# Kernel optimization log

Hardware: AMD Instinct MI355X
Metric: run time of the kernel (lower is better)

Reference implementation:

```python
import jax, jax.numpy as jnp
import numpy as np

DIM = 1024
HID = 2816
E = 8
TOPK = 2
B, S = 4, 1024


def setup_inputs() -> dict:
    key = jax.random.key(0)
    k_x, k_g, k1, k2, k3 = jax.random.split(key, 5)
    scale_d = 1.0 / np.sqrt(DIM)
    scale_h = 1.0 / np.sqrt(HID)
    return {
        "x": jax.random.normal(k_x, (B, S, DIM), dtype=jnp.float32),
        "Wg": jax.random.normal(k_g, (E, DIM), dtype=jnp.float32) * scale_d,   # gate: Linear(dim, E), no bias
        "W1": jax.random.normal(k1, (E, HID, DIM), dtype=jnp.float32) * scale_d,  # swiglu gate proj
        "W3": jax.random.normal(k3, (E, HID, DIM), dtype=jnp.float32) * scale_d,  # swiglu up proj
        "W2": jax.random.normal(k2, (E, DIM, HID), dtype=jnp.float32) * scale_h,  # down proj
    }


def reference(x, Wg, W1, W3, W2):
    Bsz, Ssz, D = x.shape
    xt = x.reshape(Bsz * Ssz, D)                        # [T, D]

    # Gating: top-k over expert scores, softmax over selected logits
    scores = xt @ Wg.T                                   # [T, E]
    top_vals, top_idx = jax.lax.top_k(scores, TOPK)      # [T, K]
    weights = jax.nn.softmax(top_vals, axis=-1)          # [T, K]

    # Dense grouped SwiGLU: run every expert on every token (vectorized),
    # then gather the top-k expert outputs per token.
    h1 = jnp.einsum('td,ehd->teh', xt, W1)               # [T, E, H]
    h3 = jnp.einsum('td,ehd->teh', xt, W3)               # [T, E, H]
    expert_out = jnp.einsum('teh,edh->ted', jax.nn.silu(h1) * h3, W2)  # [T, E, D]

    # Gather per-token selected experts and combine with gate weights
    idx = top_idx[:, :, None]                            # [T, K, 1]
    sel = jnp.take_along_axis(expert_out, idx, axis=1)   # [T, K, D]
    out = jnp.sum(sel * weights[:, :, None], axis=1)     # [T, D]
    return out.reshape(Bsz, Ssz, D)
```

## Files before the change

kernel.cpp:

```cpp
#include <hip/hip_runtime.h>
#include <hip/hip_bf16.h>

#define DIM  1024
#define HID  2816
#define NE   8
#define NTOK 4096
#define NPAIR 8192
#define CAP  8192

#define NT_UP (HID / 128)
#define MT    (CAP / 128)
#define NT_DN (DIM / 128)
#define NWG_UP (NE * NT_UP * MT)
#define NWG_DN (NE * NT_DN * MT)

typedef __bf16 bf16x8 __attribute__((ext_vector_type(8)));
typedef float f32x4 __attribute__((ext_vector_type(4)));

#define OFF_CNT  0
#define OFF_LIST 1024
#define OFF_WP   (OFF_LIST + NE*CAP*4)
#define OFF_H1   (OFF_WP + NPAIR*4)
#define OFF_XB   ((size_t)1 << 20)
#define OFF_W1B  ((size_t)10 << 20)
#define OFF_W3B  ((size_t)57 << 20)
#define OFF_H2   ((size_t)106 << 20)
#define WS_NEED  (OFF_H2 + (size_t)NPAIR * HID * 2)

#define GLB(p) ((const __attribute__((address_space(1))) void*)(p))
#define LDS(p) ((__attribute__((address_space(3))) void*)(p))

__global__ __launch_bounds__(64) void gate_kernel(
    const float* __restrict__ x, const float* __restrict__ Wg,
    int* __restrict__ counts, int* __restrict__ list, float* __restrict__ wpair,
    __bf16* __restrict__ xb) {
  int t = blockIdx.x;
  int lane = threadIdx.x;
  const float* xp = x + (size_t)t * DIM;
  float xr[16];
#pragma unroll
  for (int i = 0; i < 16; ++i) xr[i] = xp[lane + 64 * i];
  if (xb) {
    __bf16* xo = xb + (size_t)t * DIM;
#pragma unroll
    for (int i = 0; i < 16; ++i) xo[lane + 64 * i] = (__bf16)xr[i];
  }
  float s[NE];
#pragma unroll
  for (int e = 0; e < NE; ++e) {
    const float* wp = Wg + e * DIM;
    float acc = 0.f;
#pragma unroll
    for (int i = 0; i < 16; ++i) acc += xr[i] * wp[lane + 64 * i];
#pragma unroll
    for (int off = 32; off >= 1; off >>= 1) acc += __shfl_xor(acc, off, 64);
    s[e] = acc;
  }
  if (lane == 0) {
    int i0 = 0; float b0 = s[0];
#pragma unroll
    for (int e = 1; e < NE; ++e) if (s[e] > b0) { b0 = s[e]; i0 = e; }
    int i1 = -1; float b1 = -1e30f;
#pragma unroll
    for (int e = 0; e < NE; ++e) if (e != i0 && s[e] > b1) { b1 = s[e]; i1 = e; }
    float e1 = __expf(b1 - b0);
    float w0 = 1.f / (1.f + e1);
    float w1 = e1 * w0;
    int s0 = atomicAdd(&counts[i0], 1);
    list[i0 * CAP + s0] = 2 * t;
    wpair[2 * t] = w0;
    int s1 = atomicAdd(&counts[i1], 1);
    list[i1 * CAP + s1] = 2 * t + 1;
    wpair[2 * t + 1] = w1;
  }
}

__global__ __launch_bounds__(256) void cvt_kernel(
    const float* __restrict__ src, __bf16* __restrict__ dst) {
  size_t i = (((size_t)blockIdx.x * 256) + threadIdx.x) * 8;
  float4 f0 = *(const float4*)(src + i);
  float4 f1 = *(const float4*)(src + i + 4);
  bf16x8 v;
  v[0] = (__bf16)f0.x; v[1] = (__bf16)f0.y; v[2] = (__bf16)f0.z; v[3] = (__bf16)f0.w;
  v[4] = (__bf16)f1.x; v[5] = (__bf16)f1.y; v[6] = (__bf16)f1.z; v[7] = (__bf16)f1.w;
  *(bf16x8*)(dst + i) = v;
}


__global__ __launch_bounds__(256, 2) void up4_kernel(
    const __bf16* __restrict__ xb, const __bf16* __restrict__ w1b,
    const __bf16* __restrict__ w3b, const int* __restrict__ counts,
    const int* __restrict__ list, const float* __restrict__ wpair,
    __bf16* __restrict__ Hbuf) {
  int bid = blockIdx.x;
  int g = (bid & 7) * (NWG_UP / 8) + (bid >> 3);
  int e = g / (NT_UP * MT);
  int rr0 = g % (NT_UP * MT);
  int cnt = counts[e];
  int m0 = (rr0 % MT) * 128;
  if (m0 >= cnt) return;
  int h0 = (rr0 / MT) * 128;

  __shared__ __bf16 As[128 * 64];
  __shared__ __bf16 B1s[128 * 64];
  __shared__ __bf16 B3s[128 * 64];

  int tid = threadIdx.x;
  int lane = tid & 63;
  int w = tid >> 6;
  int cl = lane & 15, hi = lane >> 4;
  int wr = w >> 1, wc = w & 1;
  int l8 = lane >> 3, cc = lane & 7;

  const __bf16* asrc[4];
  const __bf16* b1src[4];
  const __bf16* b3src[4];
#pragma unroll
  for (int i = 0; i < 4; ++i) {
    int r = (w * 4 + i) * 8 + l8;
    int csel = (cc ^ (r & 7)) * 8;
    int mrow = m0 + r; if (mrow > cnt - 1) mrow = cnt - 1;
    int p = list[e * CAP + mrow];
    asrc[i]  = xb + (size_t)(p >> 1) * DIM + csel;
    b1src[i] = w1b + ((size_t)e * HID + h0 + r) * DIM + csel;
    b3src[i] = w3b + ((size_t)e * HID + h0 + r) * DIM + csel;
  }

  f32x4 acc1[4][4] = {};
  f32x4 acc3[4][4] = {};

  for (int k0 = 0; k0 < DIM; k0 += 64) {
#pragma unroll
    for (int i = 0; i < 4; ++i) {
      int q = (w * 4 + i) * 1024;
      __builtin_amdgcn_global_load_lds(GLB(asrc[i] + k0),  LDS((char*)As  + q), 16, 0, 0);
      __builtin_amdgcn_global_load_lds(GLB(b1src[i] + k0), LDS((char*)B1s + q), 16, 0, 0);
      __builtin_amdgcn_global_load_lds(GLB(b3src[i] + k0), LDS((char*)B3s + q), 16, 0, 0);
    }
    __syncthreads();
#pragma unroll
    for (int ks = 0; ks < 2; ++ks) {
      int c = hi + ks * 4;
      bf16x8 a[4], bb1[4], bb3[4];
#pragma unroll
      for (int mi = 0; mi < 4; ++mi) {
        int r = wr * 64 + mi * 16 + cl;
        a[mi] = *(const bf16x8*)((const char*)As + r * 128 + ((c ^ (r & 7)) * 16));
      }
#pragma unroll
      for (int ni = 0; ni < 4; ++ni) {
        int r = wc * 64 + ni * 16 + cl;
        bb1[ni] = *(const bf16x8*)((const char*)B1s + r * 128 + ((c ^ (r & 7)) * 16));
        bb3[ni] = *(const bf16x8*)((const char*)B3s + r * 128 + ((c ^ (r & 7)) * 16));
      }
#pragma unroll
      for (int mi = 0; mi < 4; ++mi)
#pragma unroll
        for (int ni = 0; ni < 4; ++ni) {
          acc1[mi][ni] = __builtin_amdgcn_mfma_f32_16x16x32_bf16(a[mi], bb1[ni], acc1[mi][ni], 0, 0, 0);
          acc3[mi][ni] = __builtin_amdgcn_mfma_f32_16x16x32_bf16(a[mi], bb3[ni], acc3[mi][ni], 0, 0, 0);
        }
    }
    __syncthreads();
  }

#pragma unroll
  for (int mi = 0; mi < 4; ++mi) {
#pragma unroll
    for (int rr = 0; rr < 4; ++rr) {
      int m = m0 + wr * 64 + mi * 16 + hi * 4 + rr;
      if (m < cnt) {
        int p = list[e * CAP + m];
        float wgt = wpair[p];
        __bf16* hp = Hbuf + (size_t)p * HID + h0 + wc * 64 + cl;
#pragma unroll
        for (int ni = 0; ni < 4; ++ni) {
          float v1 = acc1[mi][ni][rr], v3 = acc3[mi][ni][rr];
          float gv = (v1 / (1.f + __expf(-v1))) * v3 * wgt;
          hp[ni * 16] = (__bf16)gv;
        }
      }
    }
  }
}

__global__ __launch_bounds__(256, 2) void down4_kernel(
    const __bf16* __restrict__ Hbuf, const __bf16* __restrict__ w2b,
    const int* __restrict__ counts, const int* __restrict__ list,
    __bf16* __restrict__ Obuf) {
  int bid = blockIdx.x;
  int g = (bid & 7) * (NWG_DN / 8) + (bid >> 3);
  int e = g / (NT_DN * MT);
  int rr0 = g % (NT_DN * MT);
  int cnt = counts[e];
  int m0 = (rr0 % MT) * 128;
  if (m0 >= cnt) return;
  int d0 = (rr0 / MT) * 128;

  __shared__ __bf16 As[128 * 64];
  __shared__ __bf16 Bs[128 * 64];

  int tid = threadIdx.x;
  int lane = tid & 63;
  int w = tid >> 6;
  int cl = lane & 15, hi = lane >> 4;
  int wr = w >> 1, wc = w & 1;
  int l8 = lane >> 3, cc = lane & 7;

  const __bf16* asrc[4];
  const __bf16* bsrc[4];
#pragma unroll
  for (int i = 0; i < 4; ++i) {
    int r = (w * 4 + i) * 8 + l8;
    int csel = (cc ^ (r & 7)) * 8;
    int mrow = m0 + r; if (mrow > cnt - 1) mrow = cnt - 1;
    int p = list[e * CAP + mrow];
    asrc[i] = Hbuf + (size_t)p * HID + csel;
    bsrc[i] = w2b + ((size_t)e * DIM + d0 + r) * HID + csel;
  }

  f32x4 acc[4][4] = {};

  for (int k0 = 0; k0 < HID; k0 += 64) {
#pragma unroll
    for (int i = 0; i < 4; ++i) {
      int q = (w * 4 + i) * 1024;
      __builtin_amdgcn_global_load_lds(GLB(asrc[i] + k0), LDS((char*)As + q), 16, 0, 0);
      __builtin_amdgcn_global_load_lds(GLB(bsrc[i] + k0), LDS((char*)Bs + q), 16, 0, 0);
    }
    __syncthreads();
#pragma unroll
    for (int ks = 0; ks < 2; ++ks) {
      int c = hi + ks * 4;
      bf16x8 a[4], b[4];
#pragma unroll
      for (int mi = 0; mi < 4; ++mi) {
        int r = wr * 64 + mi * 16 + cl;
        a[mi] = *(const bf16x8*)((const char*)As + r * 128 + ((c ^ (r & 7)) * 16));
      }
#pragma unroll
      for (int ni = 0; ni < 4; ++ni) {
        int r = wc * 64 + ni * 16 + cl;
        b[ni] = *(const bf16x8*)((const char*)Bs + r * 128 + ((c ^ (r & 7)) * 16));
      }
#pragma unroll
      for (int mi = 0; mi < 4; ++mi)
#pragma unroll
        for (int ni = 0; ni < 4; ++ni)
          acc[mi][ni] = __builtin_amdgcn_mfma_f32_16x16x32_bf16(a[mi], b[ni], acc[mi][ni], 0, 0, 0);
    }
    __syncthreads();
  }

#pragma unroll
  for (int mi = 0; mi < 4; ++mi) {
#pragma unroll
    for (int rr = 0; rr < 4; ++rr) {
      int m = m0 + wr * 64 + mi * 16 + hi * 4 + rr;
      if (m < cnt) {
        int p = list[e * CAP + m];
        __bf16* op = Obuf + (size_t)p * DIM + d0 + wc * 64 + cl;
#pragma unroll
        for (int ni = 0; ni < 4; ++ni)
          op[ni * 16] = (__bf16)acc[mi][ni][rr];
      }
    }
  }
}

__global__ __launch_bounds__(256) void combine_kernel(
    const __bf16* __restrict__ Obuf, float* __restrict__ out) {
  size_t j = (((size_t)blockIdx.x * 256) + threadIdx.x) * 8;
  size_t t = j >> 10;
  bf16x8 a = *(const bf16x8*)(Obuf + j + t * DIM);
  bf16x8 b = *(const bf16x8*)(Obuf + j + t * DIM + DIM);
  float4 o0, o1;
  o0.x = (float)a[0] + (float)b[0]; o0.y = (float)a[1] + (float)b[1];
  o0.z = (float)a[2] + (float)b[2]; o0.w = (float)a[3] + (float)b[3];
  o1.x = (float)a[4] + (float)b[4]; o1.y = (float)a[5] + (float)b[5];
  o1.z = (float)a[6] + (float)b[6]; o1.w = (float)a[7] + (float)b[7];
  *(float4*)(out + j) = o0;
  *(float4*)(out + j + 4) = o1;
}

__device__ __forceinline__ void cvt_store16(__bf16* dst, const float* src) {
#pragma unroll
  for (int j = 0; j < 2; ++j) {
    float4 f0 = *(const float4*)(src + j * 8);
    float4 f1 = *(const float4*)(src + j * 8 + 4);
    bf16x8 v;
    v[0] = (__bf16)f0.x; v[1] = (__bf16)f0.y; v[2] = (__bf16)f0.z; v[3] = (__bf16)f0.w;
    v[4] = (__bf16)f1.x; v[5] = (__bf16)f1.y; v[6] = (__bf16)f1.z; v[7] = (__bf16)f1.w;
    *(bf16x8*)(dst + j * 8) = v;
  }
}

__global__ __launch_bounds__(256) void up_kernel(
    const float* __restrict__ x, const float* __restrict__ W1,
    const float* __restrict__ W3, const int* __restrict__ counts,
    const int* __restrict__ list, __bf16* __restrict__ Hbuf) {
  int e = blockIdx.z;
  int cnt = counts[e];
  int m0 = blockIdx.y * 64;
  if (m0 >= cnt) return;
  int h0 = blockIdx.x * 64;

  __shared__ __bf16 As[64][72];
  __shared__ __bf16 B1s[64][72];
  __shared__ __bf16 B3s[64][72];

  int tid = threadIdx.x;
  int r = tid >> 2;
  int cs = (tid & 3) * 16;

  const float* asrc = nullptr;
  int mrow = m0 + r;
  if (mrow < cnt) {
    int p = list[e * CAP + mrow];
    asrc = x + (size_t)(p >> 1) * DIM;
  }
  const float* b1src = W1 + ((size_t)e * HID + (h0 + r)) * DIM;
  const float* b3src = W3 + ((size_t)e * HID + (h0 + r)) * DIM;

  int lane = tid & 63;
  int w = tid >> 6;
  int wr = w >> 1, wc = w & 1;
  int cl = lane & 15, hi = lane >> 4;

  f32x4 acc1[2][2] = {};
  f32x4 acc3[2][2] = {};

  for (int k0 = 0; k0 < DIM; k0 += 64) {
    if (asrc) {
      cvt_store16(&As[r][cs], asrc + k0 + cs);
    } else {
      bf16x8 z = {};
      *(bf16x8*)&As[r][cs] = z;
      *(bf16x8*)&As[r][cs + 8] = z;
    }
    cvt_store16(&B1s[r][cs], b1src + k0 + cs);
    cvt_store16(&B3s[r][cs], b3src + k0 + cs);
    __syncthreads();
#pragma unroll
    for (int ks = 0; ks < 64; ks += 32) {
      bf16x8 a[2], b1f[2], b3f[2];
#pragma unroll
      for (int mi = 0; mi < 2; ++mi)
        a[mi] = *(const bf16x8*)&As[wr * 32 + mi * 16 + cl][ks + hi * 8];
#pragma unroll
      for (int ni = 0; ni < 2; ++ni) {
        b1f[ni] = *(const bf16x8*)&B1s[wc * 32 + ni * 16 + cl][ks + hi * 8];
        b3f[ni] = *(const bf16x8*)&B3s[wc * 32 + ni * 16 + cl][ks + hi * 8];
      }
#pragma unroll
      for (int mi = 0; mi < 2; ++mi)
#pragma unroll
        for (int ni = 0; ni < 2; ++ni) {
          acc1[mi][ni] = __builtin_amdgcn_mfma_f32_16x16x32_bf16(a[mi], b1f[ni], acc1[mi][ni], 0, 0, 0);
          acc3[mi][ni] = __builtin_amdgcn_mfma_f32_16x16x32_bf16(a[mi], b3f[ni], acc3[mi][ni], 0, 0, 0);
        }
    }
    __syncthreads();
  }

#pragma unroll
  for (int mi = 0; mi < 2; ++mi) {
#pragma unroll
    for (int rr = 0; rr < 4; ++rr) {
      int m = m0 + wr * 32 + mi * 16 + hi * 4 + rr;
      if (m < cnt) {
        int p = list[e * CAP + m];
        __bf16* hp = Hbuf + (size_t)p * HID + h0 + wc * 32 + cl;
#pragma unroll
        for (int ni = 0; ni < 2; ++ni) {
          float v1 = acc1[mi][ni][rr], v3 = acc3[mi][ni][rr];
          float gg = (v1 / (1.f + __expf(-v1))) * v3;
          hp[ni * 16] = (__bf16)gg;
        }
      }
    }
  }
}

__global__ __launch_bounds__(256) void down_kernel(
    const __bf16* __restrict__ Hbuf, const float* __restrict__ W2,
    const int* __restrict__ counts, const int* __restrict__ list,
    const float* __restrict__ wpair, float* __restrict__ out) {
  int e = blockIdx.z;
  int cnt = counts[e];
  int m0 = blockIdx.y * 64;
  if (m0 >= cnt) return;
  int d0 = blockIdx.x * 64;

  __shared__ __bf16 As[64][72];
  __shared__ __bf16 Bs[64][72];

  int tid = threadIdx.x;
  int r = tid >> 2;
  int cs = (tid & 3) * 16;

  const __bf16* asrc = nullptr;
  int mrow = m0 + r;
  if (mrow < cnt) {
    int p = list[e * CAP + mrow];
    asrc = Hbuf + (size_t)p * HID;
  }
  const float* bsrc = W2 + ((size_t)e * DIM + (d0 + r)) * HID;

  int lane = tid & 63;
  int w = tid >> 6;
  int wr = w >> 1, wc = w & 1;
  int cl = lane & 15, hi = lane >> 4;

  f32x4 acc[2][2] = {};

  for (int k0 = 0; k0 < HID; k0 += 64) {
    if (asrc) {
      *(bf16x8*)&As[r][cs]     = *(const bf16x8*)(asrc + k0 + cs);
      *(bf16x8*)&As[r][cs + 8] = *(const bf16x8*)(asrc + k0 + cs + 8);
    } else {
      bf16x8 z = {};
      *(bf16x8*)&As[r][cs] = z;
      *(bf16x8*)&As[r][cs + 8] = z;
    }
    cvt_store16(&Bs[r][cs], bsrc + k0 + cs);
    __syncthreads();
#pragma unroll
    for (int ks = 0; ks < 64; ks += 32) {
      bf16x8 a[2], b[2];
#pragma unroll
      for (int mi = 0; mi < 2; ++mi)
        a[mi] = *(const bf16x8*)&As[wr * 32 + mi * 16 + cl][ks + hi * 8];
#pragma unroll
      for (int ni = 0; ni < 2; ++ni)
        b[ni] = *(const bf16x8*)&Bs[wc * 32 + ni * 16 + cl][ks + hi * 8];
#pragma unroll
      for (int mi = 0; mi < 2; ++mi)
#pragma unroll
        for (int ni = 0; ni < 2; ++ni)
          acc[mi][ni] = __builtin_amdgcn_mfma_f32_16x16x32_bf16(a[mi], b[ni], acc[mi][ni], 0, 0, 0);
    }
    __syncthreads();
  }

#pragma unroll
  for (int mi = 0; mi < 2; ++mi) {
#pragma unroll
    for (int rr = 0; rr < 4; ++rr) {
      int m = m0 + wr * 32 + mi * 16 + hi * 4 + rr;
      if (m < cnt) {
        int p = list[e * CAP + m];
        int t = p >> 1;
        float wgt = wpair[p];
        float* op = out + (size_t)t * DIM + d0 + wc * 32 + cl;
#pragma unroll
        for (int ni = 0; ni < 2; ++ni)
          atomicAdd(&op[ni * 16], wgt * acc[mi][ni][rr]);
      }
    }
  }
}

extern "C" void kernel_launch(void* const* d_in, const int* in_sizes, int n_in,
                              void* d_out, int out_size, void* d_ws, size_t ws_size,
                              hipStream_t stream) {
  const float* x  = (const float*)d_in[0];
  const float* Wg = (const float*)d_in[1];
  const float* W1 = (const float*)d_in[2];
  const float* W3 = (const float*)d_in[3];
  const float* W2 = (const float*)d_in[4];
  float* out = (float*)d_out;

  char* ws = (char*)d_ws;
  int* counts  = (int*)(ws + OFF_CNT);
  int* list    = (int*)(ws + OFF_LIST);
  float* wpair = (float*)(ws + OFF_WP);

  hipMemsetAsync(counts, 0, 64, stream);

  if (ws_size >= WS_NEED) {
    __bf16* xb   = (__bf16*)(ws + OFF_XB);
    __bf16* w1b  = (__bf16*)(ws + OFF_W1B);
    __bf16* w3b  = (__bf16*)(ws + OFF_W3B);
    __bf16* Hbuf = (__bf16*)(ws + OFF_H2);
    __bf16* Obuf = (__bf16*)(ws + OFF_W3B);

    gate_kernel<<<NTOK, 64, 0, stream>>>(x, Wg, counts, list, wpair, xb);

    cvt_kernel<<<NE * HID * DIM / 2048, 256, 0, stream>>>(W1, w1b);
    cvt_kernel<<<NE * HID * DIM / 2048, 256, 0, stream>>>(W3, w3b);

    up4_kernel<<<NWG_UP, 256, 0, stream>>>(xb, w1b, w3b, counts, list, wpair, Hbuf);

    cvt_kernel<<<NE * DIM * HID / 2048, 256, 0, stream>>>(W2, w1b);

    down4_kernel<<<NWG_DN, 256, 0, stream>>>(Hbuf, w1b, counts, list, Obuf);

    combine_kernel<<<NTOK * DIM / 2048, 256, 0, stream>>>(Obuf, out);
  } else {
    hipMemsetAsync(d_out, 0, (size_t)out_size * sizeof(float), stream);
    __bf16* Hbuf = (__bf16*)(ws + OFF_H1);
    gate_kernel<<<NTOK, 64, 0, stream>>>(x, Wg, counts, list, wpair, nullptr);
    up_kernel<<<dim3(HID / 64, CAP / 64, NE), 256, 0, stream>>>(x, W1, W3, counts, list, Hbuf);
    down_kernel<<<dim3(DIM / 64, CAP / 64, NE), 256, 0, stream>>>(Hbuf, W2, counts, list, wpair, out);
  }
}
```

Before: 391.3 us.

## Fuse W1/W3 bf16 conversion into weight-stationary up kernel, triple-buffer down GEMM

The up projection now loads each expert's 16-row slice of fp32 W1/W3 once, converts it to bf16 in LDS, and loops over all token tiles of that expert, streaming the activations from global memory with register prefetch. This removes the two separate W1/W3 conversion passes and their bf16 copies. The down kernel uses 128x64 tiles with a three-stage global_load_lds pipeline using explicit waitcnt and barriers. In exchange, up tiles are small (16 columns), so MFMA reuse is low and activations are re-read from global for every h-slice.

```diff
diff --git a/kernel.cpp b/kernel.cpp
--- a/kernel.cpp
+++ b/kernel.cpp
@@ -8,12 +8,6 @@
 #define NPAIR 8192
 #define CAP  8192
 
-#define NT_UP (HID / 128)
-#define MT    (CAP / 128)
-#define NT_DN (DIM / 128)
-#define NWG_UP (NE * NT_UP * MT)
-#define NWG_DN (NE * NT_DN * MT)
-
 typedef __bf16 bf16x8 __attribute__((ext_vector_type(8)));
 typedef float f32x4 __attribute__((ext_vector_type(4)));
 
@@ -22,13 +16,20 @@
 #define OFF_WP   (OFF_LIST + NE*CAP*4)
 #define OFF_H1   (OFF_WP + NPAIR*4)
 #define OFF_XB   ((size_t)1 << 20)
-#define OFF_W1B  ((size_t)10 << 20)
-#define OFF_W3B  ((size_t)57 << 20)
-#define OFF_H2   ((size_t)106 << 20)
-#define WS_NEED  (OFF_H2 + (size_t)NPAIR * HID * 2)
+#define OFF_W2B  ((size_t)10 << 20)
+#define OFF_H2   ((size_t)57 << 20)
+#define OFF_OB   ((size_t)104 << 20)
+#define WS_NEED  (OFF_OB + (size_t)NPAIR * DIM * 2)
 
 #define GLB(p) ((const __attribute__((address_space(1))) void*)(p))
 #define LDS(p) ((__attribute__((address_space(3))) void*)(p))
+
+__device__ __forceinline__ bf16x8 pack8(float4 a, float4 b) {
+  bf16x8 v;
+  v[0] = (__bf16)a.x; v[1] = (__bf16)a.y; v[2] = (__bf16)a.z; v[3] = (__bf16)a.w;
+  v[4] = (__bf16)b.x; v[5] = (__bf16)b.y; v[6] = (__bf16)b.z; v[7] = (__bf16)b.w;
+  return v;
+}
 
 __global__ __launch_bounds__(64) void gate_kernel(
     const float* __restrict__ x, const float* __restrict__ Wg,
@@ -80,88 +81,205 @@
   size_t i = (((size_t)blockIdx.x * 256) + threadIdx.x) * 8;
   float4 f0 = *(const float4*)(src + i);
   float4 f1 = *(const float4*)(src + i + 4);
-  bf16x8 v;
-  v[0] = (__bf16)f0.x; v[1] = (__bf16)f0.y; v[2] = (__bf16)f0.z; v[3] = (__bf16)f0.w;
-  v[4] = (__bf16)f1.x; v[5] = (__bf16)f1.y; v[6] = (__bf16)f1.z; v[7] = (__bf16)f1.w;
-  *(bf16x8*)(dst + i) = v;
-}
-
-
-__global__ __launch_bounds__(256, 2) void up4_kernel(
-    const __bf16* __restrict__ xb, const __bf16* __restrict__ w1b,
-    const __bf16* __restrict__ w3b, const int* __restrict__ counts,
+  *(bf16x8*)(dst + i) = pack8(f0, f1);
+}
+
+__global__ __launch_bounds__(256) void up7_kernel(
+    const __bf16* __restrict__ xb, const float* __restrict__ W1,
+    const float* __restrict__ W3, const int* __restrict__ counts,
     const int* __restrict__ list, const float* __restrict__ wpair,
     __bf16* __restrict__ Hbuf) {
-  int bid = blockIdx.x;
-  int g = (bid & 7) * (NWG_UP / 8) + (bid >> 3);
-  int e = g / (NT_UP * MT);
-  int rr0 = g % (NT_UP * MT);
+  int g = blockIdx.x;
+  int e = g / (HID / 16);
+  int h0 = (g % (HID / 16)) * 16;
   int cnt = counts[e];
-  int m0 = (rr0 % MT) * 128;
-  if (m0 >= cnt) return;
-  int h0 = (rr0 / MT) * 128;
-
-  __shared__ __bf16 As[128 * 64];
-  __shared__ __bf16 B1s[128 * 64];
-  __shared__ __bf16 B3s[128 * 64];
+
+  __shared__ __bf16 B1s[16 * 1024];
+  __shared__ __bf16 B3s[16 * 1024];
 
   int tid = threadIdx.x;
   int lane = tid & 63;
   int w = tid >> 6;
   int cl = lane & 15, hi = lane >> 4;
+
+  {
+    int row = tid >> 4;
+    const float* w1p = W1 + ((size_t)e * HID + h0 + row) * DIM;
+    const float* w3p = W3 + ((size_t)e * HID + h0 + row) * DIM;
+#pragma unroll
+    for (int i = 0; i < 8; ++i) {
+      int c16 = (tid & 15) + 16 * i;
+      int dst = row * 2048 + ((c16 ^ (row & 7)) * 16);
+      float4 a0 = *(const float4*)(w1p + c16 * 8);
+      float4 a1 = *(const float4*)(w1p + c16 * 8 + 4);
+      *(bf16x8*)((char*)B1s + dst) = pack8(a0, a1);
+      float4 b0 = *(const float4*)(w3p + c16 * 8);
+      float4 b1v = *(const float4*)(w3p + c16 * 8 + 4);
+      *(bf16x8*)((char*)B3s + dst) = pack8(b0, b1v);
+    }
+  }
+  __syncthreads();
+
+  int nmt = (cnt + 127) >> 7;
+  const int* lste = list + e * CAP;
+
+  for (int mt = 0; mt < nmt; ++mt) {
+    int m0 = mt * 128;
+    size_t apos[2];
+#pragma unroll
+    for (int mi = 0; mi < 2; ++mi) {
+      int r = m0 + w * 32 + mi * 16 + cl;
+      if (r > cnt - 1) r = cnt - 1;
+      int p = lste[r];
+      apos[mi] = (size_t)(p >> 1) * DIM + hi * 8;
+    }
+
+    f32x4 acc1[2] = {};
+    f32x4 acc3[2] = {};
+
+    bf16x8 af[2][2][2];
+#pragma unroll
+    for (int kt = 0; kt < 2; ++kt)
+#pragma unroll
+      for (int mi = 0; mi < 2; ++mi)
+#pragma unroll
+        for (int ks = 0; ks < 2; ++ks)
+          af[kt][mi][ks] = *(const bf16x8*)(xb + apos[mi] + kt * 64 + ks * 32);
+
+#pragma unroll
+    for (int kt = 0; kt < 16; ++kt) {
+      int par = kt & 1;
+      bf16x8 b1f[2], b3f[2];
+#pragma unroll
+      for (int ks = 0; ks < 2; ++ks) {
+        int c16 = kt * 8 + ks * 4 + hi;
+        int off = cl * 2048 + ((c16 ^ (cl & 7)) * 16);
+        b1f[ks] = *(const bf16x8*)((const char*)B1s + off);
+        b3f[ks] = *(const bf16x8*)((const char*)B3s + off);
+      }
+#pragma unroll
+      for (int ks = 0; ks < 2; ++ks)
+#pragma unroll
+        for (int mi = 0; mi < 2; ++mi) {
+          acc1[mi] = __builtin_amdgcn_mfma_f32_16x16x32_bf16(af[par][mi][ks], b1f[ks], acc1[mi], 0, 0, 0);
+          acc3[mi] = __builtin_amdgcn_mfma_f32_16x16x32_bf16(af[par][mi][ks], b3f[ks], acc3[mi], 0, 0, 0);
+        }
+      if (kt + 2 < 16) {
+#pragma unroll
+        for (int mi = 0; mi < 2; ++mi)
+#pragma unroll
+          for (int ks = 0; ks < 2; ++ks)
+            af[par][mi][ks] = *(const bf16x8*)(xb + apos[mi] + (kt + 2) * 64 + ks * 32);
+      }
+    }
+
+#pragma unroll
+    for (int mi = 0; mi < 2; ++mi) {
+#pragma unroll
+      for (int rr = 0; rr < 4; ++rr) {
+        int m = m0 + w * 32 + mi * 16 + hi * 4 + rr;
+        if (m < cnt) {
+          int p = lste[m];
+          float wgt = wpair[p];
+          float v1 = acc1[mi][rr], v3 = acc3[mi][rr];
+          float gv = (v1 / (1.f + __expf(-v1))) * v3 * wgt;
+          Hbuf[(size_t)p * HID + h0 + cl] = (__bf16)gv;
+        }
+      }
+    }
+  }
+}
+
+__global__ __launch_bounds__(256, 2) void down6_kernel(
+    const __bf16* __restrict__ Hbuf, const __bf16* __restrict__ w2b,
+    const int* __restrict__ counts, const int* __restrict__ list,
+    __bf16* __restrict__ Obuf) {
+  int g = blockIdx.x;
+  int e = g >> 8;
+  int rem = g & 255;
+  int m0 = (rem & 15) * 128;
+  int d0 = (rem >> 4) * 64;
+  int cnt = counts[e];
+  if (m0 >= cnt) return;
+
+  __shared__ __bf16 As[3][128 * 64];
+  __shared__ __bf16 Bs[3][64 * 64];
+
+  int tid = threadIdx.x;
+  int lane = tid & 63;
+  int w = tid >> 6;
   int wr = w >> 1, wc = w & 1;
-  int l8 = lane >> 3, cc = lane & 7;
+  int cl = lane & 15, hi = lane >> 4;
 
   const __bf16* asrc[4];
-  const __bf16* b1src[4];
-  const __bf16* b3src[4];
-#pragma unroll
-  for (int i = 0; i < 4; ++i) {
-    int r = (w * 4 + i) * 8 + l8;
-    int csel = (cc ^ (r & 7)) * 8;
-    int mrow = m0 + r; if (mrow > cnt - 1) mrow = cnt - 1;
-    int p = list[e * CAP + mrow];
-    asrc[i]  = xb + (size_t)(p >> 1) * DIM + csel;
-    b1src[i] = w1b + ((size_t)e * HID + h0 + r) * DIM + csel;
-    b3src[i] = w3b + ((size_t)e * HID + h0 + r) * DIM + csel;
-  }
-
-  f32x4 acc1[4][4] = {};
-  f32x4 acc3[4][4] = {};
-
-  for (int k0 = 0; k0 < DIM; k0 += 64) {
+  const __bf16* bsrc[2];
+  {
+    int cc = tid & 7;
 #pragma unroll
     for (int i = 0; i < 4; ++i) {
-      int q = (w * 4 + i) * 1024;
-      __builtin_amdgcn_global_load_lds(GLB(asrc[i] + k0),  LDS((char*)As  + q), 16, 0, 0);
-      __builtin_amdgcn_global_load_lds(GLB(b1src[i] + k0), LDS((char*)B1s + q), 16, 0, 0);
-      __builtin_amdgcn_global_load_lds(GLB(b3src[i] + k0), LDS((char*)B3s + q), 16, 0, 0);
-    }
-    __syncthreads();
-#pragma unroll
-    for (int ks = 0; ks < 2; ++ks) {
-      int c = hi + ks * 4;
-      bf16x8 a[4], bb1[4], bb3[4];
-#pragma unroll
-      for (int mi = 0; mi < 4; ++mi) {
-        int r = wr * 64 + mi * 16 + cl;
-        a[mi] = *(const bf16x8*)((const char*)As + r * 128 + ((c ^ (r & 7)) * 16));
-      }
-#pragma unroll
-      for (int ni = 0; ni < 4; ++ni) {
-        int r = wc * 64 + ni * 16 + cl;
-        bb1[ni] = *(const bf16x8*)((const char*)B1s + r * 128 + ((c ^ (r & 7)) * 16));
-        bb3[ni] = *(const bf16x8*)((const char*)B3s + r * 128 + ((c ^ (r & 7)) * 16));
-      }
-#pragma unroll
-      for (int mi = 0; mi < 4; ++mi)
-#pragma unroll
-        for (int ni = 0; ni < 4; ++ni) {
-          acc1[mi][ni] = __builtin_amdgcn_mfma_f32_16x16x32_bf16(a[mi], bb1[ni], acc1[mi][ni], 0, 0, 0);
-          acc3[mi][ni] = __builtin_amdgcn_mfma_f32_16x16x32_bf16(a[mi], bb3[ni], acc3[mi][ni], 0, 0, 0);
-        }
-    }
-    __syncthreads();
+      int r = i * 32 + (tid >> 3);
+      int csel = (cc ^ (r & 7)) * 8;
+      int mrow = m0 + r; if (mrow > cnt - 1) mrow = cnt - 1;
+      int p = list[e * CAP + mrow];
+      asrc[i] = Hbuf + (size_t)p * HID + csel;
+    }
+#pragma unroll
+    for (int i = 0; i < 2; ++i) {
+      int r = i * 32 + (tid >> 3);
+      int csel = (cc ^ (r & 7)) * 8;
+      bsrc[i] = w2b + ((size_t)e * DIM + d0 + r) * HID + csel;
+    }
+  }
+
+  f32x4 acc[4][2] = {};
+
+#define DN6_ISSUE(slot, j)                                                       \
+  { int k0 = (j) * 64;                                                           \
+    _Pragma("unroll") for (int i = 0; i < 4; ++i)                                \
+      __builtin_amdgcn_global_load_lds(GLB(asrc[i] + k0),                        \
+          LDS((char*)As + (slot) * 16384 + i * 4096 + tid * 16), 16, 0, 0);      \
+    _Pragma("unroll") for (int i = 0; i < 2; ++i)                                \
+      __builtin_amdgcn_global_load_lds(GLB(bsrc[i] + k0),                        \
+          LDS((char*)Bs + (slot) * 8192 + i * 4096 + tid * 16), 16, 0, 0); }
+
+#define DN6_COMPUTE(slot)                                                        \
+  { const char* Ab = (const char*)As + (slot) * 16384;                           \
+    const char* Bb = (const char*)Bs + (slot) * 8192;                            \
+    _Pragma("unroll") for (int ks = 0; ks < 2; ++ks) {                           \
+      int c = hi + ks * 4;                                                       \
+      bf16x8 a[4], b[2];                                                         \
+      _Pragma("unroll") for (int mi = 0; mi < 4; ++mi) {                         \
+        int r = wr * 64 + mi * 16 + cl;                                          \
+        a[mi] = *(const bf16x8*)(Ab + r * 128 + ((c ^ (r & 7)) * 16));           \
+      }                                                                          \
+      _Pragma("unroll") for (int ni = 0; ni < 2; ++ni) {                         \
+        int r = wc * 32 + ni * 16 + cl;                                          \
+        b[ni] = *(const bf16x8*)(Bb + r * 128 + ((c ^ (r & 7)) * 16));           \
+      }                                                                          \
+      _Pragma("unroll") for (int mi = 0; mi < 4; ++mi)                           \
+        _Pragma("unroll") for (int ni = 0; ni < 2; ++ni)                         \
+          acc[mi][ni] = __builtin_amdgcn_mfma_f32_16x16x32_bf16(a[mi], b[ni], acc[mi][ni], 0, 0, 0); \
+  } }
+
+  DN6_ISSUE(0, 0)
+  DN6_ISSUE(1, 1)
+  asm volatile("s_waitcnt vmcnt(6)" ::: "memory");
+  asm volatile("s_barrier" ::: "memory");
+
+  int sc = 0;
+#pragma unroll 1
+  for (int j = 0; j < HID / 64; ++j) {
+    int si = sc + 2; if (si >= 3) si -= 3;
+    if (j < HID / 64 - 2) { DN6_ISSUE(si, j + 2) }
+    __builtin_amdgcn_sched_barrier(0);
+    DN6_COMPUTE(sc)
+    if (j < HID / 64 - 2) {
+      asm volatile("s_waitcnt vmcnt(6)" ::: "memory");
+    } else {
+      asm volatile("s_waitcnt vmcnt(0)" ::: "memory");
+    }
+    asm volatile("s_barrier" ::: "memory");
+    ++sc; if (sc == 3) sc = 0;
   }
 
 #pragma unroll
@@ -171,97 +289,9 @@
       int m = m0 + wr * 64 + mi * 16 + hi * 4 + rr;
       if (m < cnt) {
         int p = list[e * CAP + m];
-        float wgt = wpair[p];
-        __bf16* hp = Hbuf + (size_t)p * HID + h0 + wc * 64 + cl;
-#pragma unroll
-        for (int ni = 0; ni < 4; ++ni) {
-          float v1 = acc1[mi][ni][rr], v3 = acc3[mi][ni][rr];
-          float gv = (v1 / (1.f + __expf(-v1))) * v3 * wgt;
-          hp[ni * 16] = (__bf16)gv;
-        }
-      }
-    }
-  }
-}
-
-__global__ __launch_bounds__(256, 2) void down4_kernel(
-    const __bf16* __restrict__ Hbuf, const __bf16* __restrict__ w2b,
-    const int* __restrict__ counts, const int* __restrict__ list,
-    __bf16* __restrict__ Obuf) {
-  int bid = blockIdx.x;
-  int g = (bid & 7) * (NWG_DN / 8) + (bid >> 3);
-  int e = g / (NT_DN * MT);
-  int rr0 = g % (NT_DN * MT);
-  int cnt = counts[e];
-  int m0 = (rr0 % MT) * 128;
-  if (m0 >= cnt) return;
-  int d0 = (rr0 / MT) * 128;
-
-  __shared__ __bf16 As[128 * 64];
-  __shared__ __bf16 Bs[128 * 64];
-
-  int tid = threadIdx.x;
-  int lane = tid & 63;
-  int w = tid >> 6;
-  int cl = lane & 15, hi = lane >> 4;
-  int wr = w >> 1, wc = w & 1;
-  int l8 = lane >> 3, cc = lane & 7;
-
-  const __bf16* asrc[4];
-  const __bf16* bsrc[4];
-#pragma unroll
-  for (int i = 0; i < 4; ++i) {
-    int r = (w * 4 + i) * 8 + l8;
-    int csel = (cc ^ (r & 7)) * 8;
-    int mrow = m0 + r; if (mrow > cnt - 1) mrow = cnt - 1;
-    int p = list[e * CAP + mrow];
-    asrc[i] = Hbuf + (size_t)p * HID + csel;
-    bsrc[i] = w2b + ((size_t)e * DIM + d0 + r) * HID + csel;
-  }
-
-  f32x4 acc[4][4] = {};
-
-  for (int k0 = 0; k0 < HID; k0 += 64) {
-#pragma unroll
-    for (int i = 0; i < 4; ++i) {
-      int q = (w * 4 + i) * 1024;
-      __builtin_amdgcn_global_load_lds(GLB(asrc[i] + k0), LDS((char*)As + q), 16, 0, 0);
-      __builtin_amdgcn_global_load_lds(GLB(bsrc[i] + k0), LDS((char*)Bs + q), 16, 0, 0);
-    }
-    __syncthreads();
-#pragma unroll
-    for (int ks = 0; ks < 2; ++ks) {
-      int c = hi + ks * 4;
-      bf16x8 a[4], b[4];
-#pragma unroll
-      for (int mi = 0; mi < 4; ++mi) {
-        int r = wr * 64 + mi * 16 + cl;
-        a[mi] = *(const bf16x8*)((const char*)As + r * 128 + ((c ^ (r & 7)) * 16));
-      }
-#pragma unroll
-      for (int ni = 0; ni < 4; ++ni) {
-        int r = wc * 64 + ni * 16 + cl;
-        b[ni] = *(const bf16x8*)((const char*)Bs + r * 128 + ((c ^ (r & 7)) * 16));
-      }
-#pragma unroll
-      for (int mi = 0; mi < 4; ++mi)
-#pragma unroll
-        for (int ni = 0; ni < 4; ++ni)
-          acc[mi][ni] = __builtin_amdgcn_mfma_f32_16x16x32_bf16(a[mi], b[ni], acc[mi][ni], 0, 0, 0);
-    }
-    __syncthreads();
-  }
-
-#pragma unroll
-  for (int mi = 0; mi < 4; ++mi) {
-#pragma unroll
-    for (int rr = 0; rr < 4; ++rr) {
-      int m = m0 + wr * 64 + mi * 16 + hi * 4 + rr;
-      if (m < cnt) {
-        int p = list[e * CAP + m];
-        __bf16* op = Obuf + (size_t)p * DIM + d0 + wc * 64 + cl;
-#pragma unroll
-        for (int ni = 0; ni < 4; ++ni)
+        __bf16* op = Obuf + (size_t)p * DIM + d0 + wc * 32 + cl;
+#pragma unroll
+        for (int ni = 0; ni < 2; ++ni)
           op[ni * 16] = (__bf16)acc[mi][ni][rr];
       }
     }
@@ -288,10 +318,7 @@
   for (int j = 0; j < 2; ++j) {
     float4 f0 = *(const float4*)(src + j * 8);
     float4 f1 = *(const float4*)(src + j * 8 + 4);
-    bf16x8 v;
-    v[0] = (__bf16)f0.x; v[1] = (__bf16)f0.y; v[2] = (__bf16)f0.z; v[3] = (__bf16)f0.w;
-    v[4] = (__bf16)f1.x; v[5] = (__bf16)f1.y; v[6] = (__bf16)f1.z; v[7] = (__bf16)f1.w;
-    *(bf16x8*)(dst + j * 8) = v;
+    *(bf16x8*)(dst + j * 8) = pack8(f0, f1);
   }
 }
 
@@ -480,21 +507,17 @@
 
   if (ws_size >= WS_NEED) {
     __bf16* xb   = (__bf16*)(ws + OFF_XB);
-    __bf16* w1b  = (__bf16*)(ws + OFF_W1B);
-    __bf16* w3b  = (__bf16*)(ws + OFF_W3B);
+    __bf16* w2b  = (__bf16*)(ws + OFF_W2B);
     __bf16* Hbuf = (__bf16*)(ws + OFF_H2);
-    __bf16* Obuf = (__bf16*)(ws + OFF_W3B);
+    __bf16* Obuf = (__bf16*)(ws + OFF_OB);
 
     gate_kernel<<<NTOK, 64, 0, stream>>>(x, Wg, counts, list, wpair, xb);
 
-    cvt_kernel<<<NE * HID * DIM / 2048, 256, 0, stream>>>(W1, w1b);
-    cvt_kernel<<<NE * HID * DIM / 2048, 256, 0, stream>>>(W3, w3b);
-
-    up4_kernel<<<NWG_UP, 256, 0, stream>>>(xb, w1b, w3b, counts, list, wpair, Hbuf);
-
-    cvt_kernel<<<NE * DIM * HID / 2048, 256, 0, stream>>>(W2, w1b);
-
-    down4_kernel<<<NWG_DN, 256, 0, stream>>>(Hbuf, w1b, counts, list, Obuf);
+    cvt_kernel<<<NE * DIM * HID / 2048, 256, 0, stream>>>(W2, w2b);
+
+    up7_kernel<<<NE * (HID / 16), 256, 0, stream>>>(xb, W1, W3, counts, list, wpair, Hbuf);
+
+    down6_kernel<<<NE * 256, 256, 0, stream>>>(Hbuf, w2b, counts, list, Obuf);
 
     combine_kernel<<<NTOK * DIM / 2048, 256, 0, stream>>>(Obuf, out);
   } else {
```

Result: slower. 1.161 ms (+196.8%).
